# Kernel tuning notes

Measured on AMD Instinct MI355X. Metric: run time of the kernel, lower is better.

Reference implementation:

```python
import jax, jax.numpy as jnp
import numpy as np

N = 4096
IN_DIM = 256
H = 4        # n_heads
D = 64       # head_dim (out_dim)
NEG_SLOPE = 0.2


def setup_inputs() -> dict:
    key = jax.random.key(0)
    k_h, k_adj, k_zero, k_W, k_a = jax.random.split(key, 5)
    h = jax.random.normal(k_h, (N, IN_DIM), dtype=jnp.float32)
    adj = jax.random.normal(k_adj, (N, N), dtype=jnp.float32)
    keep = jax.random.uniform(k_zero, (N, N)) >= 0.3
    adj_bias = jnp.where(keep, adj, 0.0)
    W = jax.random.normal(k_W, (IN_DIM, H * D), dtype=jnp.float32) * 0.05
    a = jax.random.normal(k_a, (H, 2 * D), dtype=jnp.float32) * 0.05
    return {"h": h, "adj_bias": adj_bias, "W": W, "a": a}


def reference(h, adj_bias, W, a):
    n = h.shape[0]
    Wh = (h @ W).reshape(n, H, D)                       # [N, H, D]
    # (cat([Wh_i, Wh_j]) * a).sum(-1) separates into two rank-1 terms:
    a_i, a_j = a[:, :D], a[:, D:]                       # [H, D] each
    e_i = jnp.einsum('nhd,hd->nh', Wh, a_i)             # score from dest node i
    e_j = jnp.einsum('nhd,hd->nh', Wh, a_j)             # score from src node j
    e = jax.nn.leaky_relu(e_i[:, None, :] + e_j[None, :, :], NEG_SLOPE)  # [N,N,H]
    mask = (adj_bias == 0.0)[:, :, None]                # [N, N, 1]
    e = e + adj_bias[:, :, None]
    e = jnp.where(mask, -jnp.inf, e)
    # rows where every neighbor is masked: force self-loop score 0
    all_masked = jnp.all(mask, axis=1, keepdims=True)   # [N, 1, 1]
    self_loop = jnp.eye(n, dtype=bool)[:, :, None]      # [N, N, 1]
    e = jnp.where(all_masked & self_loop, 0.0, e)
    alpha = jax.nn.softmax(e, axis=1)                   # softmax over sources j
    # dropout: eval mode (p acts as identity), faithful to training=False
    out = jnp.einsum('ijh,jhd->ihd', alpha, Wh).reshape(n, H * D)  # concat heads
    return jax.nn.elu(out)
```

## Files before the change

kernel.cpp:

```cpp
#include <hip/hip_runtime.h>
#include <cstdint>
#include <cstddef>


typedef _Float16 f16x4 __attribute__((ext_vector_type(4)));
typedef _Float16 f16x8 __attribute__((ext_vector_type(8)));
typedef float f32x4 __attribute__((ext_vector_type(4)));

#define NN 4096

__global__ __launch_bounds__(256) void gemm_wh(
    const float* __restrict__ A, const float* __restrict__ Bw,
    const float* __restrict__ av, float* __restrict__ C,
    _Float16* __restrict__ Vt,
    _Float16* __restrict__ uit, _Float16* __restrict__ ui5t,
    _Float16* __restrict__ ujt, _Float16* __restrict__ uj5t) {
  __shared__ float sA[32][36];
  __shared__ float sB[32][68];
  __shared__ _Float16 sT[64][40];
  const int h  = blockIdx.x;
  const int by = blockIdx.y;
  const int t  = threadIdx.x;
  const int row0 = by * 32, col0 = h * 64;
  const int tc = t & 15, tr = t >> 4;
  float acc[2][4];
  #pragma unroll
  for (int q = 0; q < 2; q++)
    #pragma unroll
    for (int p = 0; p < 4; p++) acc[q][p] = 0.f;

  for (int k0 = 0; k0 < 256; k0 += 32) {
    __syncthreads();
    {
      const int r = t >> 3, k4 = (t & 7) * 4;
      float4 v = *(const float4*)&A[(size_t)(row0 + r) * 256 + k0 + k4];
      sA[k4 + 0][r] = v.x; sA[k4 + 1][r] = v.y;
      sA[k4 + 2][r] = v.z; sA[k4 + 3][r] = v.w;
    }
    #pragma unroll
    for (int q = 0; q < 2; q++) {
      const int u = t + q * 256;
      const int kr = u >> 4, c4 = (u & 15) * 4;
      *(float4*)&sB[kr][c4] =
          *(const float4*)&Bw[(size_t)(k0 + kr) * 256 + col0 + c4];
    }
    __syncthreads();
    #pragma unroll
    for (int kk = 0; kk < 32; kk++) {
      float2 a2 = *(const float2*)&sA[kk][tr * 2];
      float4 bv = *(const float4*)&sB[kk][tc * 4];
      const float bp[4] = {bv.x, bv.y, bv.z, bv.w};
      #pragma unroll
      for (int p = 0; p < 4; p++) {
        acc[0][p] = fmaf(a2.x, bp[p], acc[0][p]);
        acc[1][p] = fmaf(a2.y, bp[p], acc[1][p]);
      }
    }
  }
  #pragma unroll
  for (int q = 0; q < 2; q++) {
    float4 v = make_float4(acc[q][0], acc[q][1], acc[q][2], acc[q][3]);
    *(float4*)&C[(size_t)(row0 + tr * 2 + q) * 256 + col0 + tc * 4] = v;
  }
  {
    float pi[2] = {0.f, 0.f}, pj[2] = {0.f, 0.f};
    #pragma unroll
    for (int q = 0; q < 2; q++)
      #pragma unroll
      for (int p = 0; p < 4; p++) {
        const int d = tc * 4 + p;
        pi[q] = fmaf(acc[q][p], av[h * 128 + d], pi[q]);
        pj[q] = fmaf(acc[q][p], av[h * 128 + 64 + d], pj[q]);
      }
    #pragma unroll
    for (int m = 1; m <= 8; m <<= 1) {
      #pragma unroll
      for (int q = 0; q < 2; q++) {
        pi[q] += __shfl_xor(pi[q], m, 64);
        pj[q] += __shfl_xor(pj[q], m, 64);
      }
    }
    if (tc == 0) {
      #pragma unroll
      for (int q = 0; q < 2; q++) {
        const int row = row0 + tr * 2 + q;
        uit [(size_t)h * NN + row] = (_Float16)__expf(0.2f * pi[q]);
        ui5t[(size_t)h * NN + row] = (_Float16)__expf(pi[q]);
        ujt [(size_t)h * NN + row] = (_Float16)__expf(0.2f * pj[q]);
        uj5t[(size_t)h * NN + row] = (_Float16)__expf(pj[q]);
      }
    }
  }
  #pragma unroll
  for (int q = 0; q < 2; q++)
    #pragma unroll
    for (int p = 0; p < 4; p++)
      sT[tc * 4 + p][tr * 2 + q] = (_Float16)acc[q][p];
  __syncthreads();
  {
    const int dd = t >> 2, j8 = (t & 3) * 8;
    f16x8 w;
    #pragma unroll
    for (int k = 0; k < 8; k++) w[k] = sT[dd][j8 + k];
    *(f16x8*)&Vt[(size_t)(col0 + dd) * NN + row0 + j8] = w;
  }
}

__global__ __launch_bounds__(256, 4) void gat_attn(
    const float* __restrict__ bias, const _Float16* __restrict__ Vt,
    const _Float16* __restrict__ uit, const _Float16* __restrict__ ui5t,
    const _Float16* __restrict__ ujt, const _Float16* __restrict__ uj5t,
    float* __restrict__ P, float* __restrict__ L, int jpc) {
  __shared__ _Float16 seb[2][32][136];
  const int itile = blockIdx.x;
  const int chunk = blockIdx.y;
  const int tid = threadIdx.x;
  const int lane = tid & 63;
  const int h = __builtin_amdgcn_readfirstlane(tid >> 6);
  const int m = lane & 15;
  const int quad = lane >> 4;
  const int i0 = itile * 32;
  const int j0 = chunk * jpc;
  const int nc = jpc >> 7;

  f32x4 acc[2][5];
  #pragma unroll
  for (int it = 0; it < 2; it++)
    #pragma unroll
    for (int dt = 0; dt < 5; dt++)
      #pragma unroll
      for (int r = 0; r < 4; r++) acc[it][dt][r] = 0.f;

  const _Float16 ui_0 = uit [(size_t)h * NN + i0 + m];
  const _Float16 ui_1 = uit [(size_t)h * NN + i0 + 16 + m];
  const _Float16 u5_0 = ui5t[(size_t)h * NN + i0 + m];
  const _Float16 u5_1 = ui5t[(size_t)h * NN + i0 + 16 + m];
  const f16x8 ui8_0 = {ui_0, ui_0, ui_0, ui_0, ui_0, ui_0, ui_0, ui_0};
  const f16x8 ui8_1 = {ui_1, ui_1, ui_1, ui_1, ui_1, ui_1, ui_1, ui_1};
  const f16x8 u58_0 = {u5_0, u5_0, u5_0, u5_0, u5_0, u5_0, u5_0, u5_0};
  const f16x8 u58_1 = {u5_1, u5_1, u5_1, u5_1, u5_1, u5_1, u5_1, u5_1};
  const f16x8 kOne = {(_Float16)1.f, (_Float16)1.f, (_Float16)1.f, (_Float16)1.f,
                      (_Float16)1.f, (_Float16)1.f, (_Float16)1.f, (_Float16)1.f};

  auto stage = [&](int jc, int buf) {
    const int r = tid >> 3, f = tid & 7;
    const float* bp = bias + (size_t)(i0 + r) * NN + j0 + jc * 128;
    #pragma unroll
    for (int q = 0; q < 4; q++) {
      float4 v = *(const float4*)(bp + f * 4 + q * 32);
      f16x4 e;
      e[0] = (_Float16)((v.x == 0.f) ? 0.f : __expf(v.x));
      e[1] = (_Float16)((v.y == 0.f) ? 0.f : __expf(v.y));
      e[2] = (_Float16)((v.z == 0.f) ? 0.f : __expf(v.z));
      e[3] = (_Float16)((v.w == 0.f) ? 0.f : __expf(v.w));
      *(f16x4*)&seb[buf][r][f * 4 + q * 32] = e;
    }
  };

  stage(0, 0);
  for (int jc = 0; jc < nc; jc++) {
    const int buf = jc & 1;
    __syncthreads();
    if (jc + 1 < nc) stage(jc + 1, buf ^ 1);

    const _Float16* vb  = Vt + (size_t)(h * 64 + m) * NN + j0 + jc * 128 + quad * 8;
    const _Float16* ujb = ujt  + (size_t)h * NN + j0 + jc * 128 + quad * 8;
    const _Float16* u5b = uj5t + (size_t)h * NN + j0 + jc * 128 + quad * 8;

    f16x8 bc[4], bn[4];
    #pragma unroll
    for (int dt = 0; dt < 4; dt++)
      bc[dt] = *(const f16x8*)(vb + (size_t)(dt * 16) * NN);

    #pragma unroll
    for (int s = 0; s < 4; s++) {
      if (s < 3) {
        #pragma unroll
        for (int dt = 0; dt < 4; dt++)
          bn[dt] = *(const f16x8*)(vb + (size_t)(dt * 16) * NN + (s + 1) * 32);
      }
      const f16x8 uj8  = *(const f16x8*)(ujb + s * 32);
      const f16x8 uj58 = *(const f16x8*)(u5b + s * 32);
      const f16x8 e0 = *(const f16x8*)&seb[buf][m][s * 32 + quad * 8];
      const f16x8 e1 = *(const f16x8*)&seb[buf][m + 16][s * 32 + quad * 8];
      const f16x8 a0 = e0 * __builtin_elementwise_max(u58_0 * uj58, ui8_0 * uj8);
      const f16x8 a1 = e1 * __builtin_elementwise_max(u58_1 * uj58, ui8_1 * uj8);
      #pragma unroll
      for (int dt = 0; dt < 4; dt++) {
        acc[0][dt] = __builtin_amdgcn_mfma_f32_16x16x32_f16(a0, bc[dt], acc[0][dt], 0, 0, 0);
        acc[1][dt] = __builtin_amdgcn_mfma_f32_16x16x32_f16(a1, bc[dt], acc[1][dt], 0, 0, 0);
      }
      acc[0][4] = __builtin_amdgcn_mfma_f32_16x16x32_f16(a0, kOne, acc[0][4], 0, 0, 0);
      acc[1][4] = __builtin_amdgcn_mfma_f32_16x16x32_f16(a1, kOne, acc[1][4], 0, 0, 0);
      if (s < 3) {
        #pragma unroll
        for (int dt = 0; dt < 4; dt++) bc[dt] = bn[dt];
      }
    }
  }

  const size_t lb = (size_t)(chunk * 4 + h) * NN + i0;
  if (m == 0) {
    #pragma unroll
    for (int it = 0; it < 2; it++)
      #pragma unroll
      for (int r = 0; r < 4; r++)
        L[lb + it * 16 + quad * 4 + r] = acc[it][4][r];
  }
  const size_t pbase = ((size_t)(chunk * 4 + h) * NN + i0) * 64;
  #pragma unroll
  for (int it = 0; it < 2; it++)
    #pragma unroll
    for (int dt = 0; dt < 4; dt++)
      #pragma unroll
      for (int r = 0; r < 4; r++)
        P[pbase + (size_t)(it * 16 + quad * 4 + r) * 64 + dt * 16 + m] = acc[it][dt][r];
}

template <int CHT>
__global__ __launch_bounds__(256) void reduce_out(
    const float* __restrict__ P, const float* __restrict__ L,
    const float* __restrict__ Wh, float* __restrict__ out) {
  const int i0 = blockIdx.x * 16;
  const int h = blockIdx.y;
  const int t = threadIdx.x;
  const int d = t & 63;
  const int isub = t >> 6;
  #pragma unroll
  for (int ii = 0; ii < 4; ii++) {
    const int i = i0 + isub * 4 + ii;
    float lsum = 0.f, s = 0.f;
    #pragma unroll
    for (int c = 0; c < CHT; c++) {
      lsum += L[(size_t)(c * 4 + h) * NN + i];
      s += P[((size_t)(c * 4 + h) * NN + i) * 64 + d];
    }
    const float wh = Wh[(size_t)i * 256 + h * 64 + d];
    const bool fb = (lsum == 0.f);
    float o = fb ? wh : s / lsum;
    o = (o > 0.f) ? o : (__expf(o) - 1.f);
    out[(size_t)i * 256 + h * 64 + d] = o;
  }
}

extern "C" void kernel_launch(void* const* d_in, const int* in_sizes, int n_in,
                              void* d_out, int out_size, void* d_ws, size_t ws_size,
                              hipStream_t stream) {
  const float* h_in = (const float*)d_in[0];
  const float* adj  = (const float*)d_in[1];
  const float* W    = (const float*)d_in[2];
  const float* a    = (const float*)d_in[3];
  float* out = (float*)d_out;
  float* ws = (float*)d_ws;

  int CH = 8;
  while (CH > 1) {
    size_t floats = 1048576  + 524288  + 32768  +
                    (size_t)CH * (16384 + 1048576);
    if (floats * 4 <= ws_size) break;
    CH >>= 1;
  }
  const int jpc = NN / CH;

  float* Wh = ws;
  _Float16* Vt   = (_Float16*)(ws + 1048576);
  _Float16* uit  = (_Float16*)(ws + 1048576 + 524288);
  _Float16* ui5t = uit + 16384;
  _Float16* ujt  = ui5t + 16384;
  _Float16* uj5t = ujt + 16384;
  float* Lb = ws + 1048576 + 524288 + 32768;
  float* Pb = Lb + (size_t)CH * 16384;

  hipLaunchKernelGGL(gemm_wh, dim3(4, 128), dim3(256), 0, stream,
                     h_in, W, a, Wh, Vt, uit, ui5t, ujt, uj5t);
  hipLaunchKernelGGL(gat_attn, dim3(128, CH), dim3(256), 0, stream,
                     adj, Vt, uit, ui5t, ujt, uj5t, Pb, Lb, jpc);
  switch (CH) {
    case 8: hipLaunchKernelGGL((reduce_out<8>), dim3(256, 4), dim3(256), 0, stream, Pb, Lb, Wh, out); break;
    case 4: hipLaunchKernelGGL((reduce_out<4>), dim3(256, 4), dim3(256), 0, stream, Pb, Lb, Wh, out); break;
    case 2: hipLaunchKernelGGL((reduce_out<2>), dim3(256, 4), dim3(256), 0, stream, Pb, Lb, Wh, out); break;
    default: hipLaunchKernelGGL((reduce_out<1>), dim3(256, 4), dim3(256), 0, stream, Pb, Lb, Wh, out); break;
  }
}
```

Measured before the change: 155.1 us.

## Prefetch adj chunk into registers, vectorize reduce, raise split count to 16

The attention kernel now issues global loads for the next adjacency chunk into registers before the MFMA loop and converts them to exp'd fp16 in shared memory after the loop, so load latency overlaps with compute. The per-step V fragment double-buffering is replaced by loading V directly each step. The reduce kernel uses float2 loads and stores, and the j-split count rises from 8 to 16 when workspace allows. More splits add parallelism but double the partial-sum traffic and reduce work.

```diff
diff --git a/kernel.cpp b/kernel.cpp
--- a/kernel.cpp
+++ b/kernel.cpp
@@ -142,43 +142,47 @@
   const f16x8 kOne = {(_Float16)1.f, (_Float16)1.f, (_Float16)1.f, (_Float16)1.f,
                       (_Float16)1.f, (_Float16)1.f, (_Float16)1.f, (_Float16)1.f};
 
-  auto stage = [&](int jc, int buf) {
-    const int r = tid >> 3, f = tid & 7;
-    const float* bp = bias + (size_t)(i0 + r) * NN + j0 + jc * 128;
+  const int sr = tid >> 3, sf = tid & 7;
+  const float* bp0 = bias + (size_t)(i0 + sr) * NN + j0 + sf * 4;
+  float4 pf0, pf1, pf2, pf3;
+  auto load_chunk = [&](int jc) {
+    const float* bp = bp0 + jc * 128;
+    pf0 = *(const float4*)(bp);
+    pf1 = *(const float4*)(bp + 32);
+    pf2 = *(const float4*)(bp + 64);
+    pf3 = *(const float4*)(bp + 96);
+  };
+  auto fill = [&](int buf) {
+    float4 pv[4] = {pf0, pf1, pf2, pf3};
     #pragma unroll
     for (int q = 0; q < 4; q++) {
-      float4 v = *(const float4*)(bp + f * 4 + q * 32);
       f16x4 e;
-      e[0] = (_Float16)((v.x == 0.f) ? 0.f : __expf(v.x));
-      e[1] = (_Float16)((v.y == 0.f) ? 0.f : __expf(v.y));
-      e[2] = (_Float16)((v.z == 0.f) ? 0.f : __expf(v.z));
-      e[3] = (_Float16)((v.w == 0.f) ? 0.f : __expf(v.w));
-      *(f16x4*)&seb[buf][r][f * 4 + q * 32] = e;
+      e[0] = (_Float16)((pv[q].x == 0.f) ? 0.f : __expf(pv[q].x));
+      e[1] = (_Float16)((pv[q].y == 0.f) ? 0.f : __expf(pv[q].y));
+      e[2] = (_Float16)((pv[q].z == 0.f) ? 0.f : __expf(pv[q].z));
+      e[3] = (_Float16)((pv[q].w == 0.f) ? 0.f : __expf(pv[q].w));
+      *(f16x4*)&seb[buf][sr][sf * 4 + q * 32] = e;
     }
   };
 
-  stage(0, 0);
+  load_chunk(0);
+  fill(0);
+
   for (int jc = 0; jc < nc; jc++) {
     const int buf = jc & 1;
+    if (jc + 1 < nc) load_chunk(jc + 1);
     __syncthreads();
-    if (jc + 1 < nc) stage(jc + 1, buf ^ 1);
 
     const _Float16* vb  = Vt + (size_t)(h * 64 + m) * NN + j0 + jc * 128 + quad * 8;
     const _Float16* ujb = ujt  + (size_t)h * NN + j0 + jc * 128 + quad * 8;
     const _Float16* u5b = uj5t + (size_t)h * NN + j0 + jc * 128 + quad * 8;
 
-    f16x8 bc[4], bn[4];
-    #pragma unroll
-    for (int dt = 0; dt < 4; dt++)
-      bc[dt] = *(const f16x8*)(vb + (size_t)(dt * 16) * NN);
-
     #pragma unroll
     for (int s = 0; s < 4; s++) {
-      if (s < 3) {
-        #pragma unroll
-        for (int dt = 0; dt < 4; dt++)
-          bn[dt] = *(const f16x8*)(vb + (size_t)(dt * 16) * NN + (s + 1) * 32);
-      }
+      f16x8 bc[4];
+      #pragma unroll
+      for (int dt = 0; dt < 4; dt++)
+        bc[dt] = *(const f16x8*)(vb + (size_t)(dt * 16) * NN + s * 32);
       const f16x8 uj8  = *(const f16x8*)(ujb + s * 32);
       const f16x8 uj58 = *(const f16x8*)(u5b + s * 32);
       const f16x8 e0 = *(const f16x8*)&seb[buf][m][s * 32 + quad * 8];
@@ -192,11 +196,8 @@
       }
       acc[0][4] = __builtin_amdgcn_mfma_f32_16x16x32_f16(a0, kOne, acc[0][4], 0, 0, 0);
       acc[1][4] = __builtin_amdgcn_mfma_f32_16x16x32_f16(a1, kOne, acc[1][4], 0, 0, 0);
-      if (s < 3) {
-        #pragma unroll
-        for (int dt = 0; dt < 4; dt++) bc[dt] = bn[dt];
-      }
-    }
+    }
+    if (jc + 1 < nc) fill(buf ^ 1);
   }
 
   const size_t lb = (size_t)(chunk * 4 + h) * NN + i0;
@@ -224,22 +225,27 @@
   const int i0 = blockIdx.x * 16;
   const int h = blockIdx.y;
   const int t = threadIdx.x;
-  const int d = t & 63;
-  const int isub = t >> 6;
-  #pragma unroll
-  for (int ii = 0; ii < 4; ii++) {
-    const int i = i0 + isub * 4 + ii;
-    float lsum = 0.f, s = 0.f;
+  const int d2 = (t & 31) * 2;
+  const int isub = t >> 5;
+  #pragma unroll
+  for (int ii = 0; ii < 2; ii++) {
+    const int i = i0 + isub * 2 + ii;
+    float lsum = 0.f;
+    float sx = 0.f, sy = 0.f;
     #pragma unroll
     for (int c = 0; c < CHT; c++) {
       lsum += L[(size_t)(c * 4 + h) * NN + i];
-      s += P[((size_t)(c * 4 + h) * NN + i) * 64 + d];
-    }
-    const float wh = Wh[(size_t)i * 256 + h * 64 + d];
+      const float2 p = *(const float2*)&P[((size_t)(c * 4 + h) * NN + i) * 64 + d2];
+      sx += p.x; sy += p.y;
+    }
+    const float2 wh = *(const float2*)&Wh[(size_t)i * 256 + h * 64 + d2];
     const bool fb = (lsum == 0.f);
-    float o = fb ? wh : s / lsum;
-    o = (o > 0.f) ? o : (__expf(o) - 1.f);
-    out[(size_t)i * 256 + h * 64 + d] = o;
+    float ox = fb ? wh.x : sx / lsum;
+    float oy = fb ? wh.y : sy / lsum;
+    ox = (ox > 0.f) ? ox : (__expf(ox) - 1.f);
+    oy = (oy > 0.f) ? oy : (__expf(oy) - 1.f);
+    float2 o = make_float2(ox, oy);
+    *(float2*)&out[(size_t)i * 256 + h * 64 + d2] = o;
   }
 }
 
@@ -253,7 +259,7 @@
   float* out = (float*)d_out;
   float* ws = (float*)d_ws;
 
-  int CH = 8;
+  int CH = 16;
   while (CH > 1) {
     size_t floats = 1048576  + 524288  + 32768  +
                     (size_t)CH * (16384 + 1048576);
@@ -276,6 +282,7 @@
   hipLaunchKernelGGL(gat_attn, dim3(128, CH), dim3(256), 0, stream,
                      adj, Vt, uit, ui5t, ujt, uj5t, Pb, Lb, jpc);
   switch (CH) {
+    case 16: hipLaunchKernelGGL((reduce_out<16>), dim3(256, 4), dim3(256), 0, stream, Pb, Lb, Wh, out); break;
     case 8: hipLaunchKernelGGL((reduce_out<8>), dim3(256, 4), dim3(256), 0, stream, Pb, Lb, Wh, out); break;
     case 4: hipLaunchKernelGGL((reduce_out<4>), dim3(256, 4), dim3(256), 0, stream, Pb, Lb, Wh, out); break;
     case 2: hipLaunchKernelGGL((reduce_out<2>), dim3(256, 4), dim3(256), 0, stream, Pb, Lb, Wh, out); break;
```

Result: slower. 187.5 us (+20.9%).
